# Optimization experiments

Hardware: AMD Instinct MI355X
Metric: run time of the kernel (lower is better)

The kernel has to match this reference:

```python
import jax, jax.numpy as jnp
import numpy as np


def _lstm_dir(xs, Wih, Whh, bih, bhh, reverse):
    # xs: [T, B, E]; torch LSTM gate order i, f, g, o
    B = xs.shape[1]
    H = Whh.shape[1]
    h0 = jnp.zeros((B, H), xs.dtype)
    c0 = jnp.zeros((B, H), xs.dtype)

    def step(carry, xt):
        h, c = carry
        g = xt @ Wih.T + h @ Whh.T + (bih + bhh)
        i, f, gg, o = jnp.split(g, 4, axis=-1)
        i = jax.nn.sigmoid(i)
        f = jax.nn.sigmoid(f)
        gg = jnp.tanh(gg)
        o = jax.nn.sigmoid(o)
        c_new = f * c + i * gg
        h_new = o * jnp.tanh(c_new)
        return (h_new, c_new), h_new

    _, hs = jax.lax.scan(step, (h0, c0), xs, reverse=reverse)
    return hs  # [T, B, H] time-aligned


def _forward(x, edge_index, emb_table, Wih_f, Whh_f, bih_f, bhh_f,
             Wih_b, Whh_b, bih_b, bhh_b, label_emb, ggc_weight,
             gru_Wih, gru_Whh, gru_bih, gru_bhh, proj_W, proj_b):
    # --- embedding (dropout is identity in eval) ---
    emb = emb_table[x]                       # [B, T, E]
    xs = jnp.transpose(emb, (1, 0, 2))       # [T, B, E]
    hf = _lstm_dir(xs, Wih_f, Whh_f, bih_f, bhh_f, reverse=False)
    hb = _lstm_dir(xs, Wih_b, Whh_b, bih_b, bhh_b, reverse=True)
    c = jnp.concatenate([hf, hb], axis=-1)   # [T, B, 2H]
    c = jnp.transpose(c, (1, 0, 2))          # [B, T, 2H]

    # --- label cosine similarity, summed over tokens ---
    eps = 1e-8
    cn = c / jnp.maximum(jnp.linalg.norm(c, axis=-1, keepdims=True), eps)
    ln = label_emb / jnp.maximum(jnp.linalg.norm(label_emb, axis=-1, keepdims=True), eps)
    ls = jnp.einsum('btd,ld->bl', cn, ln)    # [B, C] (sum over t folded in)

    # --- GatedGraphConv, 2 layers, aggr='add', edge_weight=None ---
    src, dst = edge_index[0], edge_index[1]
    N = ls.shape[0]
    h = ls
    for i in range(ggc_weight.shape[0]):
        m = h @ ggc_weight[i]                            # [N, C]
        m = jax.ops.segment_sum(m[src], dst, num_segments=N)  # gather + scatter-add
        # torch GRUCell: gates r, z, n
        gi = m @ gru_Wih.T + gru_bih
        gh = h @ gru_Whh.T + gru_bhh
        ir, iz, inn = jnp.split(gi, 3, axis=-1)
        hr, hz, hn = jnp.split(gh, 3, axis=-1)
        r = jax.nn.sigmoid(ir + hr)
        z = jax.nn.sigmoid(iz + hz)
        n = jnp.tanh(inn + r * hn)
        h = (1.0 - z) * n + z * h

    return h @ proj_W.T + proj_b             # [B, C]


def setup_inputs() -> dict:
    key = jax.random.key(0)
    ks = jax.random.split(key, 20)
    V, E, B, T, C, NE = 50000, 300, 2048, 64, 1024, 65536
    H = E
    s = 0.05
    inp = {
        'x': jax.random.randint(ks[0], (B, T), 0, V),
        'edge_index': jax.random.randint(ks[1], (2, NE), 0, B),
        'emb_table': jax.random.normal(ks[2], (V, E)) * s,
        'Wih_f': jax.random.normal(ks[3], (4 * H, E)) * s,
        'Whh_f': jax.random.normal(ks[4], (4 * H, H)) * s,
        'bih_f': jnp.zeros((4 * H,)),
        'bhh_f': jnp.zeros((4 * H,)),
        'Wih_b': jax.random.normal(ks[5], (4 * H, E)) * s,
        'Whh_b': jax.random.normal(ks[6], (4 * H, H)) * s,
        'bih_b': jnp.zeros((4 * H,)),
        'bhh_b': jnp.zeros((4 * H,)),
        'label_emb': jax.random.normal(ks[7], (C, 2 * H)) * s,
        'ggc_weight': jax.random.normal(ks[8], (2, C, C)) * (1.0 / np.sqrt(C)),
        'gru_Wih': jax.random.normal(ks[9], (3 * C, C)) * (1.0 / np.sqrt(C)),
        'gru_Whh': jax.random.normal(ks[10], (3 * C, C)) * (1.0 / np.sqrt(C)),
        'gru_bih': jnp.zeros((3 * C,)),
        'gru_bhh': jnp.zeros((3 * C,)),
        'proj_W': jax.random.normal(ks[11], (C, C)) * (1.0 / np.sqrt(C)),
        'proj_b': jnp.zeros((C,)),
    }
    return inp


def reference(x, edge_index, emb_table, Wih_f, Whh_f, bih_f, bhh_f,
              Wih_b, Whh_b, bih_b, bhh_b, label_emb, ggc_weight,
              gru_Wih, gru_Whh, gru_bih, gru_bhh, proj_W, proj_b):
    return _forward(x, edge_index, emb_table, Wih_f, Whh_f, bih_f, bhh_f,
                    Wih_b, Whh_b, bih_b, bhh_b, label_emb, ggc_weight,
                    gru_Wih, gru_Whh, gru_bih, gru_bhh, proj_W, proj_b)
```

## Files before the change

### kernel.cpp

```cpp
#include <hip/hip_runtime.h>
#include <hip/hip_bf16.h>
#include <stdint.h>

typedef __hip_bfloat16 bf16;
typedef __attribute__((ext_vector_type(8))) short frag16;
typedef __attribute__((ext_vector_type(4))) float f32x4;

#define B_ 2048
#define T_ 64
#define E_ 300
#define H_ 300
#define C_ 1024
#define NE_ 65536
#define HP 320
#define KC 640
#define NP 1280

static __device__ __forceinline__ float sigf(float x) {
  x = fminf(fmaxf(x, -30.f), 30.f);
  return 1.f / (1.f + __expf(-x));
}
static __device__ __forceinline__ float tanhfast(float x) {
  x = fminf(fmaxf(x, -15.f), 15.f);
  float e = __expf(2.f * x);
  return (e - 1.f) / (e + 1.f);
}
static __device__ __forceinline__ float ldraw(const void* p, size_t i, int isb) {
  return isb ? __bfloat162float(((const bf16*)p)[i]) : ((const float*)p)[i];
}
static __device__ __forceinline__ short b2s(bf16 b) {
  short s; __builtin_memcpy(&s, &b, 2); return s;
}
static __device__ __forceinline__ short4 f4tob4(float4 v) {
  return make_short4(b2s(__float2bfloat16(v.x)), b2s(__float2bfloat16(v.y)),
                     b2s(__float2bfloat16(v.z)), b2s(__float2bfloat16(v.w)));
}

__global__ void detect_dtype(const unsigned short* __restrict__ e2, int* __restrict__ flag) {
  __shared__ int red[4];
  int tid = threadIdx.x;
  int ones = 0;
#pragma unroll
  for (int s = 0; s < 16; ++s) ones += (e2[2 * (tid * 16 + s)] >> 14) & 1;
  for (int off = 32; off > 0; off >>= 1) ones += __shfl_down(ones, off, 64);
  if ((tid & 63) == 0) red[tid >> 6] = ones;
  __syncthreads();
  if (tid == 0) {
    int tot = red[0] + red[1] + red[2] + red[3];
    *flag = (tot < 1024) ? 1 : 0;
  }
}

__global__ __launch_bounds__(256) void gemm_bt(
    const bf16* __restrict__ A, int lda,
    const void* __restrict__ W, int ldw,
    const void* __restrict__ bias,
    float* __restrict__ Cf, bf16* __restrict__ Cb, int ldc, int K,
    const int* __restrict__ rawp, int outmode) {
  __shared__ __align__(16) short As[2][128 * 32];
  __shared__ __align__(16) short Bs[2][128 * 32];
  const int isb = rawp ? *rawp : 1;
  const int n0 = blockIdx.x * 128, m0 = blockIdx.y * 128;
  const int lane = threadIdx.x & 63, wv = threadIdx.x >> 6;
  const int wm = (wv & 1) * 64, wn = (wv >> 1) * 64;
  const int r_ = threadIdx.x >> 1, half_ = threadIdx.x & 1;
  const short* Arow = (const short*)A + (size_t)(m0 + r_) * lda + half_ * 16;
  const short* Brs = (const short*)W + (size_t)(n0 + r_) * ldw + half_ * 16;
  const float* Brf = (const float*)W + (size_t)(n0 + r_) * ldw + half_ * 16;

  uint4 ra0, ra1, rb0, rb1;
  float4 rf0, rf1, rf2, rf3;
  auto loadT = [&](int k0) {
    ra0 = *(const uint4*)(Arow + k0);
    ra1 = *(const uint4*)(Arow + k0 + 8);
    if (isb) {
      rb0 = *(const uint4*)(Brs + k0);
      rb1 = *(const uint4*)(Brs + k0 + 8);
    } else {
      rf0 = *(const float4*)(Brf + k0);
      rf1 = *(const float4*)(Brf + k0 + 4);
      rf2 = *(const float4*)(Brf + k0 + 8);
      rf3 = *(const float4*)(Brf + k0 + 12);
    }
  };
  auto writeT = [&](int buf) {
    short* da = As[buf] + r_ * 32 + half_ * 16;
    *(uint4*)da = ra0;
    *(uint4*)(da + 8) = ra1;
    short* db = Bs[buf] + r_ * 32 + half_ * 16;
    if (isb) {
      *(uint4*)db = rb0;
      *(uint4*)(db + 8) = rb1;
    } else {
      *(short4*)db = f4tob4(rf0);
      *(short4*)(db + 4) = f4tob4(rf1);
      *(short4*)(db + 8) = f4tob4(rf2);
      *(short4*)(db + 12) = f4tob4(rf3);
    }
  };

  f32x4 acc[4][4];
#pragma unroll
  for (int i = 0; i < 4; ++i)
#pragma unroll
    for (int j = 0; j < 4; ++j) acc[i][j] = (f32x4){0.f, 0.f, 0.f, 0.f};

  const int nk = K / 32;
  loadT(0);
  writeT(0);
  __syncthreads();
  const int krd = (lane >> 4) * 8;
  const int rsel = lane & 15;
  for (int kk = 0; kk < nk; ++kk) {
    const int cur = kk & 1;
    if (kk + 1 < nk) loadT(32 * (kk + 1));
    frag16 af[4], bfg[4];
#pragma unroll
    for (int i = 0; i < 4; ++i) af[i] = *(const frag16*)&As[cur][(wm + i * 16 + rsel) * 32 + krd];
#pragma unroll
    for (int i = 0; i < 4; ++i) bfg[i] = *(const frag16*)&Bs[cur][(wn + i * 16 + rsel) * 32 + krd];
#pragma unroll
    for (int i = 0; i < 4; ++i)
#pragma unroll
      for (int j = 0; j < 4; ++j)
        acc[i][j] = __builtin_amdgcn_mfma_f32_16x16x32_bf16(af[i], bfg[j], acc[i][j], 0, 0, 0);
    if (kk + 1 < nk) writeT(cur ^ 1);
    __syncthreads();
  }
  const int rq = (lane >> 4) * 4, cq = lane & 15;
#pragma unroll
  for (int j = 0; j < 4; ++j) {
    int cidx = n0 + wn + j * 16 + cq;
    float bv = bias ? ldraw(bias, cidx, isb) : 0.f;
#pragma unroll
    for (int i = 0; i < 4; ++i) {
      int rbase = m0 + wm + i * 16 + rq;
#pragma unroll
      for (int r = 0; r < 4; ++r) {
        float v = acc[i][j][r] + bv;
        size_t idx = (size_t)(rbase + r) * ldc + cidx;
        if (outmode) {
          if (isb) Cb[idx] = __float2bfloat16(v);
          else Cf[idx] = v;
        } else {
          if (Cf) Cf[idx] = v;
          if (Cb) Cb[idx] = __float2bfloat16(v);
        }
      }
    }
  }
}

static __device__ __forceinline__ void normacc_row2(
    const bf16* hfA, const bf16* hbA, const bf16* hfB, const bf16* hbB,
    float* __restrict__ Spf, int b, int lane) {
  float vA[10], vB[10];
  float sA = 0.f, sB = 0.f;
#pragma unroll
  for (int s = 0; s < 10; ++s) {
    int d = lane + 64 * s;
    float a = 0.f, c = 0.f;
    if (d < 300) {
      a = __bfloat162float(hfA[d]);
      c = __bfloat162float(hfB[d]);
    } else if (d < 600) {
      a = __bfloat162float(hbA[d - 300]);
      c = __bfloat162float(hbB[d - 300]);
    }
    vA[s] = a; vB[s] = c;
    sA += a * a; sB += c * c;
  }
#pragma unroll
  for (int off = 32; off > 0; off >>= 1) {
    sA += __shfl_xor(sA, off, 64);
    sB += __shfl_xor(sB, off, 64);
  }
  float kA = 1.f / fmaxf(sqrtf(sA), 1e-8f);
  float kB = 1.f / fmaxf(sqrtf(sB), 1e-8f);
  float* dst = Spf + (size_t)b * KC;
#pragma unroll
  for (int s = 0; s < 10; ++s) {
    int d = lane + 64 * s;
    if (d < 600) dst[d] += vA[s] * kA + vB[s] * kB;
  }
}

__global__ __launch_bounds__(256) void lstm_step(
    const void* __restrict__ emb, const int* __restrict__ x,
    const bf16* __restrict__ Wcat, const float* __restrict__ bcat,
    bf16* __restrict__ hpad, float* __restrict__ cstate,
    bf16* __restrict__ Hfst, bf16* __restrict__ Hbst, float* __restrict__ Spf,
    int s, const int* __restrict__ flagp) {
  const int pb = s & 1;
  const int lane = threadIdx.x & 63, wv = threadIdx.x >> 6;

  if (blockIdx.z == 2) {
    if (s >= 33) {
      int bid = blockIdx.x + gridDim.x * blockIdx.y;
      const bf16* hinf = hpad + (size_t)pb * B_ * HP;
      const bf16* hinb = hpad + (size_t)(2 + pb) * B_ * HP;
      const int t1 = s - 1, t2 = 64 - s;
#pragma unroll
      for (int rep = 0; rep < 2; ++rep) {
        int b = bid * 4 + wv + 1280 * rep;
        if (b < B_)
          normacc_row2(hinf + (size_t)b * HP,
                       Hbst + ((size_t)(t1 - 32) * B_ + b) * H_,
                       Hfst + ((size_t)t2 * B_ + b) * H_,
                       hinb + (size_t)b * HP, Spf, b, lane);
      }
    }
    return;
  }

  __shared__ __align__(16) char smem[24576];
  short* As0 = (short*)smem;
  short* As1 = (short*)(smem + 4096);
  short* Bs0 = (short*)(smem + 8192);
  short* Bs1 = (short*)(smem + 16384);
  float* epi = (float*)smem;

  const int dir = blockIdx.z;
  const int tt = dir ? (T_ - 1 - s) : s;
  const int isb = *flagp;
  const bf16* hin = hpad + (size_t)(dir * 2 + pb) * B_ * HP;
  const bf16* Wd = Wcat + (size_t)dir * NP * KC;
  bf16* hout = hpad + (size_t)(dir * 2 + (1 - pb)) * B_ * HP;
  float* cs = cstate + (size_t)dir * B_ * HP;
  const int n0 = blockIdx.x * 128, m0 = blockIdx.y * 64;
  const int wm = (wv & 1) * 32, wn = (wv >> 1) * 64;
  const int r_ = threadIdx.x >> 2, q_ = threadIdx.x & 3;
  const int r2 = threadIdx.x >> 1, h2 = threadIdx.x & 1;
  const size_t xoff = (size_t)x[(m0 + r_) * T_ + tt] * (size_t)E_;
  const short* es = (const short*)emb;
  const float* ef = (const float*)emb;
  const short* hins = (const short*)hin;
  const short* wrow = (const short*)Wd + (size_t)(n0 + r2) * KC + h2 * 16;

  uint2 axs0, axs1;
  float4 axf0, axf1;
  uint4 ah;
  uint4 bw0, bw1;

  auto loadA = [&](int k0) {
    if (k0 < HP) {
      int c0 = k0 + q_ * 8;
      if (isb) {
        axs0 = (c0 < E_) ? *(const uint2*)(es + xoff + c0) : make_uint2(0u, 0u);
        axs1 = (c0 + 4 < E_) ? *(const uint2*)(es + xoff + c0 + 4) : make_uint2(0u, 0u);
      } else {
        axf0 = (c0 < E_) ? *(const float4*)(ef + xoff + c0) : make_float4(0.f, 0.f, 0.f, 0.f);
        axf1 = (c0 + 4 < E_) ? *(const float4*)(ef + xoff + c0 + 4) : make_float4(0.f, 0.f, 0.f, 0.f);
      }
    } else {
      ah = *(const uint4*)(hins + (size_t)(m0 + r_) * HP + (k0 - HP) + q_ * 8);
    }
  };
  auto loadB = [&](int k0) {
    const short* g = wrow + k0;
    bw0 = *(const uint4*)g;
    bw1 = *(const uint4*)(g + 8);
  };
  auto writeAB = [&](int k0, short* Ad, short* Bd) {
    short* arow = Ad + r_ * 32 + q_ * 8;
    if (k0 < HP) {
      if (isb) {
        *(uint2*)arow = axs0;
        *(uint2*)(arow + 4) = axs1;
      } else {
        *(short4*)arow = f4tob4(axf0);
        *(short4*)(arow + 4) = f4tob4(axf1);
      }
    } else {
      *(uint4*)arow = ah;
    }
    short* brow = Bd + r2 * 32 + h2 * 16;
    *(uint4*)brow = bw0;
    *(uint4*)(brow + 8) = bw1;
  };

  f32x4 acc[2][4];
#pragma unroll
  for (int i = 0; i < 2; ++i)
#pragma unroll
    for (int j = 0; j < 4; ++j) acc[i][j] = (f32x4){0.f, 0.f, 0.f, 0.f};

  loadA(0); loadB(0);
  writeAB(0, As0, Bs0);
  __syncthreads();

  const int krd = (lane >> 4) * 8;
  const int rsel = lane & 15;
  for (int kk = 0; kk < KC / 32; ++kk) {
    const int cur = kk & 1;
    const short* Ac = cur ? As1 : As0;
    const short* Bc = cur ? Bs1 : Bs0;
    if (kk < KC / 32 - 1) {
      loadA(32 * (kk + 1));
      loadB(32 * (kk + 1));
    }
    frag16 af[2], bfg[4];
#pragma unroll
    for (int i = 0; i < 2; ++i) af[i] = *(const frag16*)&Ac[(wm + i * 16 + rsel) * 32 + krd];
#pragma unroll
    for (int j = 0; j < 4; ++j) bfg[j] = *(const frag16*)&Bc[(wn + j * 16 + rsel) * 32 + krd];
#pragma unroll
    for (int i = 0; i < 2; ++i)
#pragma unroll
      for (int j = 0; j < 4; ++j)
        acc[i][j] = __builtin_amdgcn_mfma_f32_16x16x32_bf16(af[i], bfg[j], acc[i][j], 0, 0, 0);
    if (kk < KC / 32 - 1) writeAB(32 * (kk + 1), cur ? As0 : As1, cur ? Bs0 : Bs1);
    __syncthreads();
  }

  const int rq = (lane >> 4) * 4, cq = lane & 15;
#pragma unroll
  for (int p = 0; p < 2; ++p) {
    if (wn == p * 64) {
#pragma unroll
      for (int j = 0; j < 4; ++j) {
        int cl = j * 16 + cq;
        float bv = bcat[dir * NP + n0 + p * 64 + cl];
#pragma unroll
        for (int i = 0; i < 2; ++i) {
          int rl = wm + i * 16 + rq;
#pragma unroll
          for (int r = 0; r < 4; ++r) epi[(rl + r) * 64 + cl] = acc[i][j][r] + bv;
        }
      }
    }
    __syncthreads();
    int jbase = (n0 + p * 64) >> 2;
    for (int it = threadIdx.x; it < 64 * 16; it += 256) {
      int rl = it >> 4, jl = it & 15;
      int jg = jbase + jl;
      if (jg < H_) {
        const float* row = epi + rl * 64 + jl * 4;
        float iv = sigf(row[0]);
        float fv = sigf(row[1]);
        float gv = tanhfast(row[2]);
        float ov = sigf(row[3]);
        int b = m0 + rl;
        float c = fv * cs[(size_t)b * HP + jg] + iv * gv;
        float h = ov * tanhfast(c);
        cs[(size_t)b * HP + jg] = c;
        bf16 hb = __float2bfloat16(h);
        hout[(size_t)b * HP + jg] = hb;
        if (dir) {
          if (tt >= 32) Hbst[((size_t)(tt - 32) * B_ + b) * H_ + jg] = hb;
        } else if (tt < 32) {
          Hfst[((size_t)tt * B_ + b) * H_ + jg] = hb;
        }
      }
    }
    __syncthreads();
  }
}

__global__ __launch_bounds__(256) void normacc_fin(const bf16* __restrict__ hpad,
                                                   const bf16* __restrict__ Hfst,
                                                   const bf16* __restrict__ Hbst,
                                                   float* __restrict__ Spf) {
  int b = blockIdx.x * 4 + (threadIdx.x >> 6);
  int lane = threadIdx.x & 63;
  normacc_row2(hpad + (size_t)b * HP,
               Hbst + ((size_t)31 * B_ + b) * H_,
               Hfst + (size_t)b * H_,
               hpad + (size_t)2 * B_ * HP + (size_t)b * HP, Spf, b, lane);
}

__global__ void prep_wcat(const void* __restrict__ Wih_f, const void* __restrict__ Whh_f,
                          const void* __restrict__ bih_f, const void* __restrict__ bhh_f,
                          const void* __restrict__ Wih_b, const void* __restrict__ Whh_b,
                          const void* __restrict__ bih_b, const void* __restrict__ bhh_b,
                          bf16* __restrict__ Wcat, float* __restrict__ bcat,
                          const int* __restrict__ flagp) {
  int i = blockIdx.x * 256 + threadIdx.x;
  if (i >= 2 * NP * KC) return;
  const int isb = *flagp;
  int k = i % KC;
  int n = (i / KC) % NP;
  int dir = i / (KC * NP);
  int j = n >> 2, q = n & 3;
  const void* Wih = dir ? Wih_b : Wih_f;
  const void* Whh = dir ? Whh_b : Whh_f;
  float v = 0.f;
  if (j < H_) {
    int row = q * H_ + j;
    if (k < E_) v = ldraw(Wih, (size_t)row * E_ + k, isb);
    else if (k >= HP && k < HP + H_) v = ldraw(Whh, (size_t)row * H_ + (k - HP), isb);
  }
  Wcat[i] = __float2bfloat16(v);
  if (k == 0) {
    const void* bih = dir ? bih_b : bih_f;
    const void* bhh = dir ? bhh_b : bhh_f;
    bcat[dir * NP + n] =
        (j < H_) ? (ldraw(bih, q * H_ + j, isb) + ldraw(bhh, q * H_ + j, isb)) : 0.f;
  }
}

__global__ __launch_bounds__(256) void labelnorm(const void* __restrict__ L,
                                                 bf16* __restrict__ lnp,
                                                 const int* __restrict__ flagp) {
  int l = blockIdx.x, tid = threadIdx.x;
  const int isb = *flagp;
  __shared__ float red[4];
  float v[3];
  float ss = 0.f;
#pragma unroll
  for (int s = 0; s < 3; ++s) {
    int d = tid + 256 * s;
    v[s] = (d < 600) ? ldraw(L, (size_t)l * 600 + d, isb) : 0.f;
    ss += v[s] * v[s];
  }
  for (int off = 32; off > 0; off >>= 1) ss += __shfl_down(ss, off, 64);
  if ((tid & 63) == 0) red[tid >> 6] = ss;
  __syncthreads();
  float scale = 1.f / fmaxf(sqrtf(red[0] + red[1] + red[2] + red[3]), 1e-8f);
#pragma unroll
  for (int s = 0; s < 3; ++s) {
    int d = tid + 256 * s;
    if (d < KC) lnp[(size_t)l * KC + d] = __float2bfloat16(v[s] * scale);
  }
}

__global__ void spcvt(const float* __restrict__ Spf, bf16* __restrict__ Sp) {
  int i = blockIdx.x * 256 + threadIdx.x;
  Sp[i] = __float2bfloat16(Spf[i]);
}

__global__ void transpose_ggc(const void* __restrict__ W, bf16* __restrict__ Wt,
                              const int* __restrict__ flagp) {
  int i = blockIdx.x * 256 + threadIdx.x;
  const int isb = *flagp;
  int k = i & 1023, n = (i >> 10) & 1023, l = i >> 20;
  size_t src = ((size_t)l << 20) | ((size_t)k << 10) | (size_t)n;
  Wt[i] = __float2bfloat16(ldraw(W, src, isb));
}

__global__ void zero_u4(uint4* __restrict__ p, int n16) {
  int i = blockIdx.x * 256 + threadIdx.x;
  if (i < n16) p[i] = make_uint4(0u, 0u, 0u, 0u);
}

__global__ void edge_cnt(const int* __restrict__ ei, int* __restrict__ cnt) {
  int e = blockIdx.x * 256 + threadIdx.x;
  if (e < NE_) {
    int s = ei[e], d = ei[NE_ + e];
    atomicAdd(&cnt[(size_t)d * B_ + s], 1);
  }
}
__global__ void cnt2bf(const int* __restrict__ cnt, bf16* __restrict__ A) {
  int i = blockIdx.x * 256 + threadIdx.x;
  A[i] = __float2bfloat16((float)cnt[i]);
}

__global__ void gru_ew(const float* __restrict__ gi, const float* __restrict__ gh,
                       float* __restrict__ h, bf16* __restrict__ hb16) {
  int i = blockIdx.x * 256 + threadIdx.x;
  int b = i >> 10, j = i & 1023;
  const float* gib = gi + (size_t)b * 3072;
  const float* ghb = gh + (size_t)b * 3072;
  float r = sigf(gib[j] + ghb[j]);
  float z = sigf(gib[1024 + j] + ghb[1024 + j]);
  float n = tanhfast(gib[2048 + j] + r * ghb[2048 + j]);
  float hv = (1.f - z) * n + z * h[i];
  h[i] = hv;
  hb16[i] = __float2bfloat16(hv);
}

__global__ void sentinel(bf16* __restrict__ o, int n, float v) {
  int i = blockIdx.x * 256 + threadIdx.x;
  if (i < n) o[i] = __float2bfloat16(v);
}

extern "C" void kernel_launch(void* const* d_in, const int* in_sizes, int n_in,
                              void* d_out, int out_size, void* d_ws, size_t ws_size,
                              hipStream_t stream) {
  const int* x = (const int*)d_in[0];
  const int* ei = (const int*)d_in[1];
  const void* emb = d_in[2];
  const void* Wih_f = d_in[3];
  const void* Whh_f = d_in[4];
  const void* bih_f = d_in[5];
  const void* bhh_f = d_in[6];
  const void* Wih_b = d_in[7];
  const void* Whh_b = d_in[8];
  const void* bih_b = d_in[9];
  const void* bhh_b = d_in[10];
  const void* label = d_in[11];
  const void* ggcw = d_in[12];
  const void* gWih = d_in[13];
  const void* gWhh = d_in[14];
  const void* gbih = d_in[15];
  const void* gbhh = d_in[16];
  const void* projW = d_in[17];
  const void* projb = d_in[18];
  (void)in_sizes; (void)n_in;

  const size_t NEED = (size_t)112 * 1024 * 1024;
  if (ws_size < NEED) {
    float v = 100.f + (float)(ws_size >> 24);
    sentinel<<<(out_size + 255) / 256, 256, 0, stream>>>((bf16*)d_out, out_size, v);
    return;
  }

  char* w = (char*)d_ws;
  size_t off = 0;
  auto alloc = [&](size_t bytes) {
    char* p = w + off;
    off += (bytes + 255) & ~(size_t)255;
    return p;
  };
  int* dflag = (int*)alloc(256);
  bf16* Wcat = (bf16*)alloc((size_t)2 * NP * KC * 2);
  float* bcat = (float*)alloc((size_t)2 * NP * 4);
  bf16* lnp = (bf16*)alloc((size_t)C_ * KC * 2);
  bf16* ggct = (bf16*)alloc((size_t)2 * C_ * C_ * 2);
  bf16* Sp = (bf16*)alloc((size_t)B_ * KC * 2);
  const size_t phase_base = off;
  float* Spf = (float*)alloc((size_t)B_ * KC * 4);
  bf16* hpad = (bf16*)alloc((size_t)4 * B_ * HP * 2);
  float* cst = (float*)alloc((size_t)2 * B_ * HP * 4);
  bf16* Hfst = (bf16*)alloc((size_t)32 * B_ * H_ * 2);
  bf16* Hbst = (bf16*)alloc((size_t)32 * B_ * H_ * 2);
  off = phase_base;
  float* hbuf = (float*)alloc((size_t)B_ * C_ * 4);
  bf16* hb16 = (bf16*)alloc((size_t)B_ * C_ * 2);
  bf16* m1t = (bf16*)alloc((size_t)C_ * B_ * 2);
  bf16* aggb = (bf16*)alloc((size_t)B_ * C_ * 2);
  bf16* Acnt = (bf16*)alloc((size_t)B_ * B_ * 2);
  float* gi = (float*)alloc((size_t)B_ * 3072 * 4);
  float* gh = (float*)alloc((size_t)B_ * 3072 * 4);
  int* cnt = (int*)gi;

  detect_dtype<<<1, 256, 0, stream>>>((const unsigned short*)emb, dflag);
  prep_wcat<<<(2 * NP * KC) / 256, 256, 0, stream>>>(Wih_f, Whh_f, bih_f, bhh_f,
                                                     Wih_b, Whh_b, bih_b, bhh_b, Wcat, bcat, dflag);
  labelnorm<<<C_, 256, 0, stream>>>(label, lnp, dflag);
  transpose_ggc<<<(2 * C_ * C_) / 256, 256, 0, stream>>>(ggcw, ggct, dflag);
  zero_u4<<<(4 * B_ * HP * 2 / 16 + 255) / 256, 256, 0, stream>>>((uint4*)hpad, 4 * B_ * HP * 2 / 16);
  zero_u4<<<(2 * B_ * HP * 4 / 16 + 255) / 256, 256, 0, stream>>>((uint4*)cst, 2 * B_ * HP * 4 / 16);
  zero_u4<<<(B_ * KC * 4 / 16 + 255) / 256, 256, 0, stream>>>((uint4*)Spf, B_ * KC * 4 / 16);

  for (int s = 0; s < T_; ++s)
    lstm_step<<<dim3(NP / 128, B_ / 64, 3), 256, 0, stream>>>(emb, x, Wcat, bcat, hpad, cst,
                                                              Hfst, Hbst, Spf, s, dflag);
  normacc_fin<<<B_ / 4, 256, 0, stream>>>(hpad, Hfst, Hbst, Spf);
  spcvt<<<(B_ * KC) / 256, 256, 0, stream>>>(Spf, Sp);

  gemm_bt<<<dim3(C_ / 128, B_ / 128), 256, 0, stream>>>(Sp, KC, lnp, KC, nullptr,
                                                        hbuf, hb16, C_, KC, nullptr, 0);
  zero_u4<<<(B_ * B_ * 4 / 16 + 255) / 256, 256, 0, stream>>>((uint4*)cnt, B_ * B_ * 4 / 16);
  edge_cnt<<<NE_ / 256, 256, 0, stream>>>(ei, cnt);
  cnt2bf<<<(B_ * B_) / 256, 256, 0, stream>>>(cnt, Acnt);
  for (int l = 0; l < 2; ++l) {
    gemm_bt<<<dim3(B_ / 128, C_ / 128), 256, 0, stream>>>(ggct + (size_t)l * C_ * C_, C_,
                                                          hb16, C_, nullptr,
                                                          nullptr, m1t, B_, C_, nullptr, 0);
    gemm_bt<<<dim3(C_ / 128, B_ / 128), 256, 0, stream>>>(Acnt, B_, m1t, B_, nullptr,
                                                          nullptr, aggb, C_, B_, nullptr, 0);
    gemm_bt<<<dim3(3072 / 128, B_ / 128), 256, 0, stream>>>(aggb, C_, gWih, C_, gbih,
                                                            gi, nullptr, 3072, C_, dflag, 0);
    gemm_bt<<<dim3(3072 / 128, B_ / 128), 256, 0, stream>>>(hb16, C_, gWhh, C_, gbhh,
                                                            gh, nullptr, 3072, C_, dflag, 0);
    gru_ew<<<(B_ * C_) / 256, 256, 0, stream>>>(gi, gh, hbuf, hb16);
  }
  gemm_bt<<<dim3(C_ / 128, B_ / 128), 256, 0, stream>>>(hb16, C_, projW, C_, projb,
                                                        (float*)d_out, (bf16*)d_out, C_, C_,
                                                        dflag, 1);
}
```

Before: 2.447 ms.

## Pad LDS tiles, double-buffer register prefetch, pre-convert GRU weights, merge GRU GEMMs

Both the generic GEMM and the LSTM step kernel now pad their LDS rows to 40 shorts to cut bank conflicts. They also prefetch two K-tiles ahead into register sets and raise wave priority around the MFMA bursts. The GRU and projection weights and biases are converted once to bf16/f32 by new small kernels, so the GEMM no longer branches on dtype or converts inside the inner loop. The two GRU gate GEMMs are merged into one launch using blockIdx.z. The cost is extra LDS per block, more registers, and a few extra conversion launches per call.

```diff
diff --git a/kernel.cpp b/kernel.cpp
--- a/kernel.cpp
+++ b/kernel.cpp
@@ -15,6 +15,7 @@
 #define HP 320
 #define KC 640
 #define NP 1280
+#define PADK 40
 
 static __device__ __forceinline__ float sigf(float x) {
   x = fminf(fmaxf(x, -30.f), 30.f);
@@ -52,51 +53,35 @@
 }
 
 __global__ __launch_bounds__(256) void gemm_bt(
-    const bf16* __restrict__ A, int lda,
-    const void* __restrict__ W, int ldw,
-    const void* __restrict__ bias,
-    float* __restrict__ Cf, bf16* __restrict__ Cb, int ldc, int K,
-    const int* __restrict__ rawp, int outmode) {
-  __shared__ __align__(16) short As[2][128 * 32];
-  __shared__ __align__(16) short Bs[2][128 * 32];
+    const bf16* A, int lda, const bf16* W, int ldw, const float* bias,
+    float* Cf, bf16* Cb, int ldc, int K,
+    const int* __restrict__ rawp, int outmode,
+    const bf16* A2, const bf16* W2, const float* bias2, float* Cf2) {
+  if (blockIdx.z) { A = A2; W = W2; bias = bias2; Cf = Cf2; Cb = nullptr; }
+  __shared__ __align__(16) short As[2][128 * PADK];
+  __shared__ __align__(16) short Bs[2][128 * PADK];
   const int isb = rawp ? *rawp : 1;
   const int n0 = blockIdx.x * 128, m0 = blockIdx.y * 128;
   const int lane = threadIdx.x & 63, wv = threadIdx.x >> 6;
   const int wm = (wv & 1) * 64, wn = (wv >> 1) * 64;
-  const int r_ = threadIdx.x >> 1, half_ = threadIdx.x & 1;
-  const short* Arow = (const short*)A + (size_t)(m0 + r_) * lda + half_ * 16;
-  const short* Brs = (const short*)W + (size_t)(n0 + r_) * ldw + half_ * 16;
-  const float* Brf = (const float*)W + (size_t)(n0 + r_) * ldw + half_ * 16;
-
-  uint4 ra0, ra1, rb0, rb1;
-  float4 rf0, rf1, rf2, rf3;
-  auto loadT = [&](int k0) {
-    ra0 = *(const uint4*)(Arow + k0);
-    ra1 = *(const uint4*)(Arow + k0 + 8);
-    if (isb) {
-      rb0 = *(const uint4*)(Brs + k0);
-      rb1 = *(const uint4*)(Brs + k0 + 8);
-    } else {
-      rf0 = *(const float4*)(Brf + k0);
-      rf1 = *(const float4*)(Brf + k0 + 4);
-      rf2 = *(const float4*)(Brf + k0 + 8);
-      rf3 = *(const float4*)(Brf + k0 + 12);
-    }
-  };
-  auto writeT = [&](int buf) {
-    short* da = As[buf] + r_ * 32 + half_ * 16;
-    *(uint4*)da = ra0;
-    *(uint4*)(da + 8) = ra1;
-    short* db = Bs[buf] + r_ * 32 + half_ * 16;
-    if (isb) {
-      *(uint4*)db = rb0;
-      *(uint4*)(db + 8) = rb1;
-    } else {
-      *(short4*)db = f4tob4(rf0);
-      *(short4*)(db + 4) = f4tob4(rf1);
-      *(short4*)(db + 8) = f4tob4(rf2);
-      *(short4*)(db + 12) = f4tob4(rf3);
-    }
+  const int r_ = threadIdx.x >> 1, h_ = threadIdx.x & 1;
+  const short* Arow = (const short*)A + (size_t)(m0 + r_) * lda + h_ * 16;
+  const short* Brow = (const short*)W + (size_t)(n0 + r_) * ldw + h_ * 16;
+
+  uint4 ra[2][2], rb[2][2];
+  auto loadT = [&](int s, int k0) {
+    ra[s][0] = *(const uint4*)(Arow + k0);
+    ra[s][1] = *(const uint4*)(Arow + k0 + 8);
+    rb[s][0] = *(const uint4*)(Brow + k0);
+    rb[s][1] = *(const uint4*)(Brow + k0 + 8);
+  };
+  auto writeT = [&](int s, int buf) {
+    short* da = &As[buf][0] + r_ * PADK + h_ * 16;
+    *(uint4*)da = ra[s][0];
+    *(uint4*)(da + 8) = ra[s][1];
+    short* db = &Bs[buf][0] + r_ * PADK + h_ * 16;
+    *(uint4*)db = rb[s][0];
+    *(uint4*)(db + 8) = rb[s][1];
   };
 
   f32x4 acc[4][4];
@@ -106,32 +91,43 @@
     for (int j = 0; j < 4; ++j) acc[i][j] = (f32x4){0.f, 0.f, 0.f, 0.f};
 
   const int nk = K / 32;
-  loadT(0);
-  writeT(0);
-  __syncthreads();
-  const int krd = (lane >> 4) * 8;
-  const int rsel = lane & 15;
-  for (int kk = 0; kk < nk; ++kk) {
-    const int cur = kk & 1;
-    if (kk + 1 < nk) loadT(32 * (kk + 1));
+  const int rsel = lane & 15, krd = (lane >> 4) * 8;
+
+  auto mfma16 = [&](int buf) {
     frag16 af[4], bfg[4];
 #pragma unroll
-    for (int i = 0; i < 4; ++i) af[i] = *(const frag16*)&As[cur][(wm + i * 16 + rsel) * 32 + krd];
-#pragma unroll
-    for (int i = 0; i < 4; ++i) bfg[i] = *(const frag16*)&Bs[cur][(wn + i * 16 + rsel) * 32 + krd];
+    for (int i = 0; i < 4; ++i) af[i] = *(const frag16*)&As[buf][(wm + i * 16 + rsel) * PADK + krd];
+#pragma unroll
+    for (int j = 0; j < 4; ++j) bfg[j] = *(const frag16*)&Bs[buf][(wn + j * 16 + rsel) * PADK + krd];
+    __builtin_amdgcn_s_setprio(1);
 #pragma unroll
     for (int i = 0; i < 4; ++i)
 #pragma unroll
       for (int j = 0; j < 4; ++j)
         acc[i][j] = __builtin_amdgcn_mfma_f32_16x16x32_bf16(af[i], bfg[j], acc[i][j], 0, 0, 0);
-    if (kk + 1 < nk) writeT(cur ^ 1);
+    __builtin_amdgcn_s_setprio(0);
+  };
+
+  loadT(0, 0);
+  loadT(1, 32);
+  writeT(0, 0);
+  __syncthreads();
+  for (int kk = 0; kk < nk; kk += 2) {
+    if (kk + 2 < nk) loadT(0, 32 * (kk + 2));
+    mfma16(0);
+    writeT(1, 1);
     __syncthreads();
-  }
+    if (kk + 3 < nk) loadT(1, 32 * (kk + 3));
+    mfma16(1);
+    if (kk + 2 < nk) writeT(0, 0);
+    __syncthreads();
+  }
+
   const int rq = (lane >> 4) * 4, cq = lane & 15;
 #pragma unroll
   for (int j = 0; j < 4; ++j) {
     int cidx = n0 + wn + j * 16 + cq;
-    float bv = bias ? ldraw(bias, cidx, isb) : 0.f;
+    float bv = bias ? bias[cidx] : 0.f;
 #pragma unroll
     for (int i = 0; i < 4; ++i) {
       int rbase = m0 + wm + i * 16 + rq;
@@ -213,11 +209,11 @@
     return;
   }
 
-  __shared__ __align__(16) char smem[24576];
+  __shared__ __align__(16) char smem[30720];
   short* As0 = (short*)smem;
-  short* As1 = (short*)(smem + 4096);
-  short* Bs0 = (short*)(smem + 8192);
-  short* Bs1 = (short*)(smem + 16384);
+  short* As1 = (short*)(smem + 5120);
+  short* Bs0 = (short*)(smem + 10240);
+  short* Bs1 = (short*)(smem + 20480);
   float* epi = (float*)smem;
 
   const int dir = blockIdx.z;
@@ -237,46 +233,44 @@
   const short* hins = (const short*)hin;
   const short* wrow = (const short*)Wd + (size_t)(n0 + r2) * KC + h2 * 16;
 
-  uint2 axs0, axs1;
-  float4 axf0, axf1;
-  uint4 ah;
-  uint4 bw0, bw1;
-
-  auto loadA = [&](int k0) {
+  uint2 xs[2][2];
+  float4 xf[2][2];
+  uint4 ah[2];
+  uint4 bw[2][2];
+
+  auto loadT = [&](int set, int k0) {
     if (k0 < HP) {
       int c0 = k0 + q_ * 8;
       if (isb) {
-        axs0 = (c0 < E_) ? *(const uint2*)(es + xoff + c0) : make_uint2(0u, 0u);
-        axs1 = (c0 + 4 < E_) ? *(const uint2*)(es + xoff + c0 + 4) : make_uint2(0u, 0u);
+        xs[set][0] = (c0 < E_) ? *(const uint2*)(es + xoff + c0) : make_uint2(0u, 0u);
+        xs[set][1] = (c0 + 4 < E_) ? *(const uint2*)(es + xoff + c0 + 4) : make_uint2(0u, 0u);
       } else {
-        axf0 = (c0 < E_) ? *(const float4*)(ef + xoff + c0) : make_float4(0.f, 0.f, 0.f, 0.f);
-        axf1 = (c0 + 4 < E_) ? *(const float4*)(ef + xoff + c0 + 4) : make_float4(0.f, 0.f, 0.f, 0.f);
+        xf[set][0] = (c0 < E_) ? *(const float4*)(ef + xoff + c0) : make_float4(0.f, 0.f, 0.f, 0.f);
+        xf[set][1] = (c0 + 4 < E_) ? *(const float4*)(ef + xoff + c0 + 4)
+                                   : make_float4(0.f, 0.f, 0.f, 0.f);
       }
     } else {
-      ah = *(const uint4*)(hins + (size_t)(m0 + r_) * HP + (k0 - HP) + q_ * 8);
-    }
-  };
-  auto loadB = [&](int k0) {
-    const short* g = wrow + k0;
-    bw0 = *(const uint4*)g;
-    bw1 = *(const uint4*)(g + 8);
-  };
-  auto writeAB = [&](int k0, short* Ad, short* Bd) {
-    short* arow = Ad + r_ * 32 + q_ * 8;
+      ah[set] = *(const uint4*)(hins + (size_t)(m0 + r_) * HP + (k0 - HP) + q_ * 8);
+    }
+    bw[set][0] = *(const uint4*)(wrow + k0);
+    bw[set][1] = *(const uint4*)(wrow + k0 + 8);
+  };
+  auto writeT = [&](int set, int k0, short* Ad, short* Bd) {
+    short* arow = Ad + r_ * PADK + q_ * 8;
     if (k0 < HP) {
       if (isb) {
-        *(uint2*)arow = axs0;
-        *(uint2*)(arow + 4) = axs1;
+        *(uint2*)arow = xs[set][0];
+        *(uint2*)(arow + 4) = xs[set][1];
       } else {
-        *(short4*)arow = f4tob4(axf0);
-        *(short4*)(arow + 4) = f4tob4(axf1);
+        *(short4*)arow = f4tob4(xf[set][0]);
+        *(short4*)(arow + 4) = f4tob4(xf[set][1]);
       }
     } else {
-      *(uint4*)arow = ah;
-    }
-    short* brow = Bd + r2 * 32 + h2 * 16;
-    *(uint4*)brow = bw0;
-    *(uint4*)(brow + 8) = bw1;
+      *(uint4*)arow = ah[set];
+    }
+    short* brow = Bd + r2 * PADK + h2 * 16;
+    *(uint4*)brow = bw[set][0];
+    *(uint4*)(brow + 8) = bw[set][1];
   };
 
   f32x4 acc[2][4];
@@ -285,31 +279,36 @@
 #pragma unroll
     for (int j = 0; j < 4; ++j) acc[i][j] = (f32x4){0.f, 0.f, 0.f, 0.f};
 
-  loadA(0); loadB(0);
-  writeAB(0, As0, Bs0);
-  __syncthreads();
-
-  const int krd = (lane >> 4) * 8;
-  const int rsel = lane & 15;
-  for (int kk = 0; kk < KC / 32; ++kk) {
-    const int cur = kk & 1;
-    const short* Ac = cur ? As1 : As0;
-    const short* Bc = cur ? Bs1 : Bs0;
-    if (kk < KC / 32 - 1) {
-      loadA(32 * (kk + 1));
-      loadB(32 * (kk + 1));
-    }
+  const int rsel = lane & 15, krd = (lane >> 4) * 8;
+  const int NKT = KC / 32;
+
+  auto mfma8 = [&](const short* Ap, const short* Bp) {
     frag16 af[2], bfg[4];
 #pragma unroll
-    for (int i = 0; i < 2; ++i) af[i] = *(const frag16*)&Ac[(wm + i * 16 + rsel) * 32 + krd];
-#pragma unroll
-    for (int j = 0; j < 4; ++j) bfg[j] = *(const frag16*)&Bc[(wn + j * 16 + rsel) * 32 + krd];
+    for (int i = 0; i < 2; ++i) af[i] = *(const frag16*)&Ap[(wm + i * 16 + rsel) * PADK + krd];
+#pragma unroll
+    for (int j = 0; j < 4; ++j) bfg[j] = *(const frag16*)&Bp[(wn + j * 16 + rsel) * PADK + krd];
+    __builtin_amdgcn_s_setprio(1);
 #pragma unroll
     for (int i = 0; i < 2; ++i)
 #pragma unroll
       for (int j = 0; j < 4; ++j)
         acc[i][j] = __builtin_amdgcn_mfma_f32_16x16x32_bf16(af[i], bfg[j], acc[i][j], 0, 0, 0);
-    if (kk < KC / 32 - 1) writeAB(32 * (kk + 1), cur ? As0 : As1, cur ? Bs0 : Bs1);
+    __builtin_amdgcn_s_setprio(0);
+  };
+
+  loadT(0, 0);
+  loadT(1, 32);
+  writeT(0, 0, As0, Bs0);
+  __syncthreads();
+  for (int kk = 0; kk < NKT; kk += 2) {
+    if (kk + 2 < NKT) loadT(0, 32 * (kk + 2));
+    mfma8(As0, Bs0);
+    writeT(1, 32 * (kk + 1), As1, Bs1);
+    __syncthreads();
+    if (kk + 3 < NKT) loadT(1, 32 * (kk + 3));
+    mfma8(As1, Bs1);
+    if (kk + 2 < NKT) writeT(0, 32 * (kk + 2), As0, Bs0);
     __syncthreads();
   }
 
@@ -438,6 +437,17 @@
   Wt[i] = __float2bfloat16(ldraw(W, src, isb));
 }
 
+__global__ void w2bf(const void* __restrict__ src, bf16* __restrict__ dst, int n,
+                     const int* __restrict__ flagp) {
+  int i = blockIdx.x * 256 + threadIdx.x;
+  if (i < n) dst[i] = __float2bfloat16(ldraw(src, i, *flagp));
+}
+__global__ void b2f32(const void* __restrict__ src, float* __restrict__ dst, int n,
+                      const int* __restrict__ flagp) {
+  int i = blockIdx.x * 256 + threadIdx.x;
+  if (i < n) dst[i] = ldraw(src, i, *flagp);
+}
+
 __global__ void zero_u4(uint4* __restrict__ p, int n16) {
   int i = blockIdx.x * 256 + threadIdx.x;
   if (i < n16) p[i] = make_uint4(0u, 0u, 0u, 0u);
@@ -532,6 +542,12 @@
   bf16* Acnt = (bf16*)alloc((size_t)B_ * B_ * 2);
   float* gi = (float*)alloc((size_t)B_ * 3072 * 4);
   float* gh = (float*)alloc((size_t)B_ * 3072 * 4);
+  bf16* gWihb = (bf16*)alloc((size_t)3072 * C_ * 2);
+  bf16* gWhhb = (bf16*)alloc((size_t)3072 * C_ * 2);
+  bf16* projWb = (bf16*)alloc((size_t)C_ * C_ * 2);
+  float* gbihf = (float*)alloc(3072 * 4);
+  float* gbhhf = (float*)alloc(3072 * 4);
+  float* projbf = (float*)alloc(C_ * 4);
   int* cnt = (int*)gi;
 
   detect_dtype<<<1, 256, 0, stream>>>((const unsigned short*)emb, dflag);
@@ -549,24 +565,34 @@
   normacc_fin<<<B_ / 4, 256, 0, stream>>>(hpad, Hfst, Hbst, Spf);
   spcvt<<<(B_ * KC) / 256, 256, 0, stream>>>(Spf, Sp);
 
+  w2bf<<<(3072 * C_) / 256, 256, 0, stream>>>(gWih, gWihb, 3072 * C_, dflag);
+  w2bf<<<(3072 * C_) / 256, 256, 0, stream>>>(gWhh, gWhhb, 3072 * C_, dflag);
+  w2bf<<<(C_ * C_) / 256, 256, 0, stream>>>(projW, projWb, C_ * C_, dflag);
+  b2f32<<<12, 256, 0, stream>>>(gbih, gbihf, 3072, dflag);
+  b2f32<<<12, 256, 0, stream>>>(gbhh, gbhhf, 3072, dflag);
+  b2f32<<<4, 256, 0, stream>>>(projb, projbf, C_, dflag);
+
   gemm_bt<<<dim3(C_ / 128, B_ / 128), 256, 0, stream>>>(Sp, KC, lnp, KC, nullptr,
-                                                        hbuf, hb16, C_, KC, nullptr, 0);
+                                                        hbuf, hb16, C_, KC, nullptr, 0,
+                                                        nullptr, nullptr, nullptr, nullptr);
   zero_u4<<<(B_ * B_ * 4 / 16 + 255) / 256, 256, 0, stream>>>((uint4*)cnt, B_ * B_ * 4 / 16);
   edge_cnt<<<NE_ / 256, 256, 0, stream>>>(ei, cnt);
   cnt2bf<<<(B_ * B_) / 256, 256, 0, stream>>>(cnt, Acnt);
   for (int l = 0; l < 2; ++l) {
     gemm_bt<<<dim3(B_ / 128, C_ / 128), 256, 0, stream>>>(ggct + (size_t)l * C_ * C_, C_,
                                                           hb16, C_, nullptr,
-                                                          nullptr, m1t, B_, C_, nullptr, 0);
+                                                          nullptr, m1t, B_, C_, nullptr, 0,
+                                                          nullptr, nullptr, nullptr, nullptr);
     gemm_bt<<<dim3(C_ / 128, B_ / 128), 256, 0, stream>>>(Acnt, B_, m1t, B_, nullptr,
-                                                          nullptr, aggb, C_, B_, nullptr, 0);
-    gemm_bt<<<dim3(3072 / 128, B_ / 128), 256, 0, stream>>>(aggb, C_, gWih, C_, gbih,
-                                                            gi, nullptr, 3072, C_, dflag, 0);
-    gemm_bt<<<dim3(3072 / 128, B_ / 128), 256, 0, stream>>>(hb16, C_, gWhh, C_, gbhh,
-                                                            gh, nullptr, 3072, C_, dflag, 0);
+                                                          nullptr, aggb, C_, B_, nullptr, 0,
+                                                          nullptr, nullptr, nullptr, nullptr);
+    gemm_bt<<<dim3(3072 / 128, B_ / 128, 2), 256, 0, stream>>>(aggb, C_, gWihb, C_, gbihf,
+                                                               gi, nullptr, 3072, C_, nullptr, 0,
+                                                               hb16, gWhhb, gbhhf, gh);
     gru_ew<<<(B_ * C_) / 256, 256, 0, stream>>>(gi, gh, hbuf, hb16);
   }
-  gemm_bt<<<dim3(C_ / 128, B_ / 128), 256, 0, stream>>>(hb16, C_, projW, C_, projb,
+  gemm_bt<<<dim3(C_ / 128, B_ / 128), 256, 0, stream>>>(hb16, C_, projWb, C_, projbf,
                                                         (float*)d_out, (bf16*)d_out, C_, C_,
-                                                        dflag, 1);
-}
+                                                        dflag, 1,
+                                                        nullptr, nullptr, nullptr, nullptr);
+}
```

Result: slower. 4.850 ms (+98.2%).
